# Kernel optimization log

Hardware: AMD Instinct MI355X
Metric: run time of the kernel (lower is better)

The kernel has to match this reference:

```python
import jax, jax.numpy as jnp
import numpy as np

KWTA = 16          # number of winners (kwta)
THRESH = 16384.0   # firing threshold


def setup_inputs() -> dict:
    key = jax.random.key(0)
    k1, k2 = jax.random.split(key)
    # SpykeTorch layout: (timesteps, in_channels, H, W)
    rec_field = jax.random.uniform(k1, (64, 1, 256, 256), dtype=jnp.float32)
    # LocalConvolution weight: kernel covers the full receptive field -> (k, C, kh, kw)
    weight = jax.random.uniform(k2, (2048, 1, 256, 256), dtype=jnp.float32)
    return {"rec_field": rec_field, "weight": weight}


def reference(rec_field, weight):
    T = rec_field.shape[0]
    K = weight.shape[0]
    # LocalConvolution with kernel == receptive field: output spatial dims are 1x1,
    # i.e. a dense projection of the flattened field onto K cells -> (T, K)
    out = jnp.einsum('tchw,kchw->tk', rec_field, weight)
    # sf.fire(out, thresh, True): threshold_ keeps values strictly > thresh, else 0
    pot = jnp.where(out > THRESH, out, jnp.zeros((), out.dtype))  # thresholded potentials
    spikes = jnp.sign(pot)                                        # 0/1 spike wave
    # sf.get_k_winners(pot, kwta, inhibition_radius=0); spikes = pot.sign()
    n_spk = spikes.sum(axis=0)                                    # (K,)
    # index of earliest spike timestep per feature, clamped to [0, T-1]
    first_idx = jnp.clip((T - n_spk).astype(jnp.int32), 0, T - 1)
    first_pot = jnp.take_along_axis(pot, first_idx[None, :], axis=0)  # (1, K)
    trunc = spikes * first_pot                                    # (T, K)
    v = trunc.max() * T                                           # large bias at spike positions
    total = (trunc + spikes * v).sum(axis=0)                      # (K,) ranking score
    # iterative argmax + zeroing of the winning feature (radius 0) == top-k,
    # with the loop's break-on-zero handled by the validity mask
    top_vals, top_idx = jax.lax.top_k(total, KWTA)
    valid = (top_vals > 0).astype(out.dtype)
    coef = jnp.zeros((K,), dtype=out.dtype).at[top_idx].set(valid)  # winner channel mask
    # coef broadcast over timesteps; restore (T, K, 1, 1) spatial layout
    return jnp.sign(pot * coef[None, :])[:, :, None, None]
```

## Files before the change

kernel.cpp:

```cpp
#include <hip/hip_runtime.h>


constexpr int KDIM   = 65536;
constexpr int NCOL   = 2048;
constexpr int TROWS  = 64;
constexpr int CTILE  = 64;
constexpr int KS     = 64;
constexpr int LDW    = KS + 4;
constexpr int KCHUNK = 4096;
constexpr double THRESH = 16384.0;

__global__ __launch_bounds__(256) void gemm_part(const float* __restrict__ A,
                                                 const float* __restrict__ W,
                                                 double* __restrict__ Cacc) {
    __shared__ float As[TROWS][LDW];
    __shared__ float Ws[CTILE][LDW];
    const int tid = threadIdx.x;
    const int cq  = tid & 15;
    const int tq  = tid >> 4;
    const int colBase = blockIdx.x * CTILE;
    const int kBase   = blockIdx.y * KCHUNK;

    double acc[4][4];
#pragma unroll
    for (int i = 0; i < 4; ++i)
#pragma unroll
        for (int c = 0; c < 4; ++c) acc[i][c] = 0.0;

    for (int ck = 0; ck < KCHUNK; ck += KS) {
        const int k0 = kBase + ck;
        __syncthreads();
#pragma unroll
        for (int it = 0; it < 4; ++it) {
            const int f  = (it * 256 + tid) * 4;
            const int r  = f >> 6;
            const int jj = f & 63;
            *(float4*)&As[r][jj] = *(const float4*)(A + (size_t)r * KDIM + k0 + jj);
            *(float4*)&Ws[r][jj] = *(const float4*)(W + (size_t)(colBase + r) * KDIM + k0 + jj);
        }
        __syncthreads();

#pragma unroll 2
        for (int j0 = 0; j0 < KS; j0 += 8) {
            float p[4][4] = {};
#pragma unroll
            for (int h = 0; h < 2; ++h) {
                const int jj = j0 + 4 * h;
                float4 av[4], wv[4];
#pragma unroll
                for (int i = 0; i < 4; ++i) av[i] = *(const float4*)&As[tq + 16 * i][jj];
#pragma unroll
                for (int c = 0; c < 4; ++c) wv[c] = *(const float4*)&Ws[cq + 16 * c][jj];
#pragma unroll
                for (int i = 0; i < 4; ++i)
#pragma unroll
                    for (int c = 0; c < 4; ++c) {
                        p[i][c] = fmaf(av[i].x, wv[c].x, p[i][c]);
                        p[i][c] = fmaf(av[i].y, wv[c].y, p[i][c]);
                        p[i][c] = fmaf(av[i].z, wv[c].z, p[i][c]);
                        p[i][c] = fmaf(av[i].w, wv[c].w, p[i][c]);
                    }
            }
#pragma unroll
            for (int i = 0; i < 4; ++i)
#pragma unroll
                for (int c = 0; c < 4; ++c) acc[i][c] += (double)p[i][c];
        }
    }

#pragma unroll
    for (int i = 0; i < 4; ++i)
#pragma unroll
        for (int c = 0; c < 4; ++c)
            atomicAdd(&Cacc[(size_t)(tq + 16 * i) * NCOL + colBase + cq + 16 * c],
                      acc[i][c]);
}

__global__ __launch_bounds__(256) void colstats(const double* __restrict__ C,
                                                int* __restrict__ nspk,
                                                double* __restrict__ fpot,
                                                unsigned long long* __restrict__ mbits) {
    const int k = blockIdx.x * blockDim.x + threadIdx.x;
    int n = 0;
    for (int t = 0; t < TROWS; ++t) n += (C[(size_t)t * NCOL + k] > THRESH) ? 1 : 0;
    int fi = TROWS - n;
    if (fi > TROWS - 1) fi = TROWS - 1;
    if (fi < 0) fi = 0;
    const double c  = C[(size_t)fi * NCOL + k];
    const double fp = (c > THRESH) ? c : 0.0;
    nspk[k] = n;
    fpot[k] = fp;
    atomicMax(mbits, (unsigned long long)__double_as_longlong(fp));
}

__global__ __launch_bounds__(256) void topk16(const double* __restrict__ fpot,
                                              const int* __restrict__ nspk,
                                              const unsigned long long* __restrict__ mbits,
                                              unsigned int* __restrict__ coef) {
    __shared__ double tot[NCOL];
    __shared__ double bv[256];
    __shared__ int    bi[256];
    const int tid = threadIdx.x;
    const double v = 64.0 * __longlong_as_double((long long)(*mbits));
    for (int k = tid; k < NCOL; k += 256)
        tot[k] = (double)nspk[k] * (fpot[k] + v);
    __syncthreads();

    for (int round = 0; round < 16; ++round) {
        double best  = -1.0;
        int    besti = 1 << 30;
        for (int k = tid; k < NCOL; k += 256) {
            const double t = tot[k];
            if (t > best || (t == best && k < besti)) { best = t; besti = k; }
        }
        bv[tid] = best;
        bi[tid] = besti;
        __syncthreads();
        for (int s = 128; s > 0; s >>= 1) {
            if (tid < s) {
                const double ov = bv[tid + s];
                const int    oi = bi[tid + s];
                if (ov > bv[tid] || (ov == bv[tid] && oi < bi[tid])) {
                    bv[tid] = ov; bi[tid] = oi;
                }
            }
            __syncthreads();
        }
        if (tid == 0) {
            const int w = bi[0];
            if (bv[0] > 0.0) coef[w] = 1u;
            tot[w] = -1.0;
        }
        __syncthreads();
    }
}

__global__ __launch_bounds__(256) void writeout(const double* __restrict__ C,
                                                const unsigned int* __restrict__ coef,
                                                float* __restrict__ out) {
    const int idx = blockIdx.x * blockDim.x + threadIdx.x;
    const int k = idx & (NCOL - 1);
    out[idx] = (coef[k] != 0u && C[idx] > THRESH) ? 1.0f : 0.0f;
}

extern "C" void kernel_launch(void* const* d_in, const int* in_sizes, int n_in,
                              void* d_out, int out_size, void* d_ws, size_t ws_size,
                              hipStream_t stream) {
    (void)in_sizes; (void)n_in; (void)out_size; (void)ws_size;
    const float* A = (const float*)d_in[0];
    const float* W = (const float*)d_in[1];
    float* out = (float*)d_out;

    char* ws = (char*)d_ws;
    double* Cacc = (double*)ws;
    double* fpot = (double*)(ws + 1048576);
    int* nspk    = (int*)(ws + 1048576 + 16384);
    unsigned long long* mbits =
        (unsigned long long*)(ws + 1048576 + 16384 + 8192);
    unsigned int* coef =
        (unsigned int*)(ws + 1048576 + 16384 + 8192 + 8);
    const size_t ws_need = 1048576 + 16384 + 8192 + 8 + 8192;

    hipMemsetAsync(d_ws, 0, ws_need, stream);

    gemm_part<<<dim3(NCOL / CTILE, KDIM / KCHUNK), 256, 0, stream>>>(A, W, Cacc);
    colstats<<<NCOL / 256, 256, 0, stream>>>(Cacc, nspk, fpot, mbits);
    topk16<<<1, 256, 0, stream>>>(fpot, nspk, mbits, coef);
    writeout<<<(TROWS * NCOL) / 256, 256, 0, stream>>>(Cacc, coef, out);
}
```

Before: 929.1 us.

## Replace FP32 FMA GEMM with exact bf16 limb-split MFMA integer accumulation

Inputs are converted to fixed-point integers (scaled by 2^23) and split into three signed 8-bit limbs stored as bf16. Nine cross-limb bf16 MFMA products per tile are accumulated in fp32, then periodically folded into 64-bit integer totals with shifts. The result is an exact integer dot product, so thresholding and top-k ranking run on integers, and ranking uses (spike count, first potential) lexicographically instead of the double-based score. The aim is to move the dominant GEMM onto matrix cores, at the cost of three times the LDS footprint, conversion work per stage, and quantisation of the inputs to 23 fractional bits.

```diff
diff --git a/kernel.cpp b/kernel.cpp
--- a/kernel.cpp
+++ b/kernel.cpp
@@ -1,146 +1,204 @@
 #include <hip/hip_runtime.h>
 
+
+typedef float  f32x4  __attribute__((ext_vector_type(4)));
+typedef __bf16 bf16x8 __attribute__((ext_vector_type(8)));
+typedef short  s16x8  __attribute__((ext_vector_type(8)));
 
 constexpr int KDIM   = 65536;
 constexpr int NCOL   = 2048;
 constexpr int TROWS  = 64;
 constexpr int CTILE  = 64;
 constexpr int KS     = 64;
-constexpr int LDW    = KS + 4;
-constexpr int KCHUNK = 4096;
-constexpr double THRESH = 16384.0;
-
-__global__ __launch_bounds__(256) void gemm_part(const float* __restrict__ A,
-                                                 const float* __restrict__ W,
-                                                 double* __restrict__ Cacc) {
-    __shared__ float As[TROWS][LDW];
-    __shared__ float Ws[CTILE][LDW];
-    const int tid = threadIdx.x;
-    const int cq  = tid & 15;
-    const int tq  = tid >> 4;
+constexpr int SPLIT  = 16;
+constexpr int KRANGE = KDIM / SPLIT;
+constexpr int STAGES = KRANGE / KS;
+constexpr int LDSTR  = 72;
+constexpr long long THRESH_I = 1LL << 60;
+
+__device__ __forceinline__ void convert_write16(const float4 v[4], short* base) {
+    const int PST = TROWS * LDSTR;
+    ushort h[3][16];
+#pragma unroll
+    for (int i = 0; i < 16; ++i) {
+        const float     x  = ((const float*)v)[i];
+        const unsigned  k  = (unsigned)(x * 8388608.0f);
+        const int       d0 = (int)((k + 128u) & 255u) - 128;
+        const unsigned  k1 = (k - (unsigned)d0) >> 8;
+        const int       d1 = (int)((k1 + 128u) & 255u) - 128;
+        const unsigned  k2 = (k1 - (unsigned)d1) >> 8;
+        h[0][i] = (ushort)(__float_as_uint((float)d0) >> 16);
+        h[1][i] = (ushort)(__float_as_uint((float)d1) >> 16);
+        h[2][i] = (ushort)(__float_as_uint((float)(int)k2) >> 16);
+    }
+#pragma unroll
+    for (int p = 0; p < 3; ++p) {
+        s16x8 lo, hi;
+#pragma unroll
+        for (int j = 0; j < 8; ++j) { lo[j] = (short)h[p][j]; hi[j] = (short)h[p][j + 8]; }
+        *(s16x8*)(base + p * PST)     = lo;
+        *(s16x8*)(base + p * PST + 8) = hi;
+    }
+}
+
+__global__ __launch_bounds__(256, 2) void gemm_limb(const float* __restrict__ A,
+                                                    const float* __restrict__ W,
+                                                    unsigned long long* __restrict__ C) {
+    __shared__ short Al[3][TROWS][LDSTR];
+    __shared__ short Wl[3][CTILE][LDSTR];
+    const int tid  = threadIdx.x;
+    const int lane = tid & 63;
+    const int wv   = tid >> 6;
+    const int r0   = (wv >> 1) * 32;
+    const int c0   = (wv & 1) * 32;
     const int colBase = blockIdx.x * CTILE;
-    const int kBase   = blockIdx.y * KCHUNK;
-
-    double acc[4][4];
-#pragma unroll
-    for (int i = 0; i < 4; ++i)
-#pragma unroll
-        for (int c = 0; c < 4; ++c) acc[i][c] = 0.0;
-
-    for (int ck = 0; ck < KCHUNK; ck += KS) {
-        const int k0 = kBase + ck;
-        __syncthreads();
-#pragma unroll
-        for (int it = 0; it < 4; ++it) {
-            const int f  = (it * 256 + tid) * 4;
-            const int r  = f >> 6;
-            const int jj = f & 63;
-            *(float4*)&As[r][jj] = *(const float4*)(A + (size_t)r * KDIM + k0 + jj);
-            *(float4*)&Ws[r][jj] = *(const float4*)(W + (size_t)(colBase + r) * KDIM + k0 + jj);
-        }
-        __syncthreads();
-
-#pragma unroll 2
-        for (int j0 = 0; j0 < KS; j0 += 8) {
-            float p[4][4] = {};
-#pragma unroll
-            for (int h = 0; h < 2; ++h) {
-                const int jj = j0 + 4 * h;
-                float4 av[4], wv[4];
-#pragma unroll
-                for (int i = 0; i < 4; ++i) av[i] = *(const float4*)&As[tq + 16 * i][jj];
-#pragma unroll
-                for (int c = 0; c < 4; ++c) wv[c] = *(const float4*)&Ws[cq + 16 * c][jj];
-#pragma unroll
-                for (int i = 0; i < 4; ++i)
-#pragma unroll
-                    for (int c = 0; c < 4; ++c) {
-                        p[i][c] = fmaf(av[i].x, wv[c].x, p[i][c]);
-                        p[i][c] = fmaf(av[i].y, wv[c].y, p[i][c]);
-                        p[i][c] = fmaf(av[i].z, wv[c].z, p[i][c]);
-                        p[i][c] = fmaf(av[i].w, wv[c].w, p[i][c]);
+    const int kBase   = blockIdx.y * KRANGE;
+
+    const int lrow  = tid >> 2;
+    const int lkoff = (tid & 3) * 16;
+
+    const int frow = lane & 15;
+    const int fk   = (lane >> 4) * 8;
+
+    f32x4 acc[5][2][2] = {};
+    long long tot[2][2][4] = {};
+
+    for (int st = 0; st < STAGES; ++st) {
+        const int k0 = kBase + st * KS;
+        float4 av[4], wv4[4];
+        const float* ap = A + (size_t)lrow * KDIM + k0 + lkoff;
+        const float* wp = W + (size_t)(colBase + lrow) * KDIM + k0 + lkoff;
+#pragma unroll
+        for (int i = 0; i < 4; ++i) av[i] = ((const float4*)ap)[i];
+#pragma unroll
+        for (int i = 0; i < 4; ++i) wv4[i] = ((const float4*)wp)[i];
+
+        __syncthreads();
+        convert_write16(av,  &Al[0][lrow][lkoff]);
+        convert_write16(wv4, &Wl[0][lrow][lkoff]);
+        __syncthreads();
+
+#pragma unroll
+        for (int ks = 0; ks < 2; ++ks) {
+            s16x8 af[3][2], bf[3][2];
+#pragma unroll
+            for (int p = 0; p < 3; ++p)
+#pragma unroll
+                for (int rt = 0; rt < 2; ++rt)
+                    af[p][rt] = *(const s16x8*)&Al[p][r0 + rt * 16 + frow][ks * 32 + fk];
+#pragma unroll
+            for (int p = 0; p < 3; ++p)
+#pragma unroll
+                for (int ct = 0; ct < 2; ++ct)
+                    bf[p][ct] = *(const s16x8*)&Wl[p][c0 + ct * 16 + frow][ks * 32 + fk];
+#pragma unroll
+            for (int p = 0; p < 3; ++p)
+#pragma unroll
+                for (int q = 0; q < 3; ++q) {
+                    const int s = p + q;
+#pragma unroll
+                    for (int rt = 0; rt < 2; ++rt)
+#pragma unroll
+                        for (int ct = 0; ct < 2; ++ct)
+                            acc[s][rt][ct] = __builtin_amdgcn_mfma_f32_16x16x32_bf16(
+                                __builtin_bit_cast(bf16x8, af[p][rt]),
+                                __builtin_bit_cast(bf16x8, bf[q][ct]),
+                                acc[s][rt][ct], 0, 0, 0);
+                }
+        }
+
+        if ((st & 3) == 3) {
+#pragma unroll
+            for (int s = 0; s < 5; ++s)
+#pragma unroll
+                for (int rt = 0; rt < 2; ++rt)
+#pragma unroll
+                    for (int ct = 0; ct < 2; ++ct) {
+#pragma unroll
+                        for (int r = 0; r < 4; ++r)
+                            tot[rt][ct][r] += ((long long)(int)acc[s][rt][ct][r]) << (8 * s);
+                        acc[s][rt][ct] = (f32x4){0.f, 0.f, 0.f, 0.f};
                     }
+        }
+    }
+
+#pragma unroll
+    for (int rt = 0; rt < 2; ++rt)
+#pragma unroll
+        for (int ct = 0; ct < 2; ++ct)
+#pragma unroll
+            for (int r = 0; r < 4; ++r) {
+                const int row = r0 + rt * 16 + (lane >> 4) * 4 + r;
+                const int col = colBase + c0 + ct * 16 + (lane & 15);
+                atomicAdd(&C[(size_t)row * NCOL + col],
+                          (unsigned long long)tot[rt][ct][r]);
             }
-#pragma unroll
-            for (int i = 0; i < 4; ++i)
-#pragma unroll
-                for (int c = 0; c < 4; ++c) acc[i][c] += (double)p[i][c];
-        }
-    }
-
-#pragma unroll
-    for (int i = 0; i < 4; ++i)
-#pragma unroll
-        for (int c = 0; c < 4; ++c)
-            atomicAdd(&Cacc[(size_t)(tq + 16 * i) * NCOL + colBase + cq + 16 * c],
-                      acc[i][c]);
-}
-
-__global__ __launch_bounds__(256) void colstats(const double* __restrict__ C,
+}
+
+__global__ __launch_bounds__(256) void colstats(const long long* __restrict__ C,
                                                 int* __restrict__ nspk,
-                                                double* __restrict__ fpot,
+                                                long long* __restrict__ fpot,
                                                 unsigned long long* __restrict__ mbits) {
     const int k = blockIdx.x * blockDim.x + threadIdx.x;
     int n = 0;
-    for (int t = 0; t < TROWS; ++t) n += (C[(size_t)t * NCOL + k] > THRESH) ? 1 : 0;
+    for (int t = 0; t < TROWS; ++t) n += (C[(size_t)t * NCOL + k] > THRESH_I) ? 1 : 0;
     int fi = TROWS - n;
     if (fi > TROWS - 1) fi = TROWS - 1;
-    if (fi < 0) fi = 0;
-    const double c  = C[(size_t)fi * NCOL + k];
-    const double fp = (c > THRESH) ? c : 0.0;
+    const long long c  = C[(size_t)fi * NCOL + k];
+    const long long fp = (c > THRESH_I) ? c : 0;
     nspk[k] = n;
     fpot[k] = fp;
-    atomicMax(mbits, (unsigned long long)__double_as_longlong(fp));
-}
-
-__global__ __launch_bounds__(256) void topk16(const double* __restrict__ fpot,
+    atomicMax(mbits, (unsigned long long)fp);
+}
+
+__global__ __launch_bounds__(256) void topk16(const long long* __restrict__ fpot,
                                               const int* __restrict__ nspk,
                                               const unsigned long long* __restrict__ mbits,
                                               unsigned int* __restrict__ coef) {
-    __shared__ double tot[NCOL];
-    __shared__ double bv[256];
-    __shared__ int    bi[256];
+    __shared__ long long sf[NCOL];
+    __shared__ int sn[NCOL];
+    __shared__ long long rv[256];
+    __shared__ int rn[256];
+    __shared__ int ri[256];
     const int tid = threadIdx.x;
-    const double v = 64.0 * __longlong_as_double((long long)(*mbits));
-    for (int k = tid; k < NCOL; k += 256)
-        tot[k] = (double)nspk[k] * (fpot[k] + v);
+    const bool anyv = (*mbits) > 0ull;
+    for (int k = tid; k < NCOL; k += 256) { sf[k] = fpot[k]; sn[k] = nspk[k]; }
     __syncthreads();
 
     for (int round = 0; round < 16; ++round) {
-        double best  = -1.0;
-        int    besti = 1 << 30;
+        int bn = -1; long long bf = -1; int bi = 1 << 30;
         for (int k = tid; k < NCOL; k += 256) {
-            const double t = tot[k];
-            if (t > best || (t == best && k < besti)) { best = t; besti = k; }
-        }
-        bv[tid] = best;
-        bi[tid] = besti;
+            const int nn = sn[k]; const long long ff = sf[k];
+            if (nn > bn || (nn == bn && (ff > bf || (ff == bf && k < bi)))) {
+                bn = nn; bf = ff; bi = k;
+            }
+        }
+        rn[tid] = bn; rv[tid] = bf; ri[tid] = bi;
         __syncthreads();
         for (int s = 128; s > 0; s >>= 1) {
             if (tid < s) {
-                const double ov = bv[tid + s];
-                const int    oi = bi[tid + s];
-                if (ov > bv[tid] || (ov == bv[tid] && oi < bi[tid])) {
-                    bv[tid] = ov; bi[tid] = oi;
+                const int on = rn[tid + s]; const long long of = rv[tid + s]; const int oi = ri[tid + s];
+                if (on > rn[tid] || (on == rn[tid] && (of > rv[tid] || (of == rv[tid] && oi < ri[tid])))) {
+                    rn[tid] = on; rv[tid] = of; ri[tid] = oi;
                 }
             }
             __syncthreads();
         }
         if (tid == 0) {
-            const int w = bi[0];
-            if (bv[0] > 0.0) coef[w] = 1u;
-            tot[w] = -1.0;
-        }
-        __syncthreads();
-    }
-}
-
-__global__ __launch_bounds__(256) void writeout(const double* __restrict__ C,
+            const int w = ri[0];
+            if (rn[0] > 0 && anyv) coef[w] = 1u;
+            sn[w] = -1;
+        }
+        __syncthreads();
+    }
+}
+
+__global__ __launch_bounds__(256) void writeout(const long long* __restrict__ C,
                                                 const unsigned int* __restrict__ coef,
                                                 float* __restrict__ out) {
     const int idx = blockIdx.x * blockDim.x + threadIdx.x;
     const int k = idx & (NCOL - 1);
-    out[idx] = (coef[k] != 0u && C[idx] > THRESH) ? 1.0f : 0.0f;
+    out[idx] = (coef[k] != 0u && C[idx] > THRESH_I) ? 1.0f : 0.0f;
 }
 
 extern "C" void kernel_launch(void* const* d_in, const int* in_sizes, int n_in,
@@ -152,18 +210,17 @@
     float* out = (float*)d_out;
 
     char* ws = (char*)d_ws;
-    double* Cacc = (double*)ws;
-    double* fpot = (double*)(ws + 1048576);
-    int* nspk    = (int*)(ws + 1048576 + 16384);
-    unsigned long long* mbits =
-        (unsigned long long*)(ws + 1048576 + 16384 + 8192);
-    unsigned int* coef =
-        (unsigned int*)(ws + 1048576 + 16384 + 8192 + 8);
-    const size_t ws_need = 1048576 + 16384 + 8192 + 8 + 8192;
-
-    hipMemsetAsync(d_ws, 0, ws_need, stream);
-
-    gemm_part<<<dim3(NCOL / CTILE, KDIM / KCHUNK), 256, 0, stream>>>(A, W, Cacc);
+    long long* Cacc = (long long*)ws;
+    unsigned long long* mbits = (unsigned long long*)(ws + 1048576);
+    unsigned int* coef = (unsigned int*)(ws + 1048576 + 8);
+    long long* fpot = (long long*)(ws + 1048576 + 8 + 8192);
+    int* nspk = (int*)(ws + 1048576 + 8 + 8192 + 16384);
+    const size_t zero_bytes = 1048576 + 8 + 8192;
+
+    hipMemsetAsync(d_ws, 0, zero_bytes, stream);
+
+    gemm_limb<<<dim3(NCOL / CTILE, SPLIT), 256, 0, stream>>>(
+        A, W, (unsigned long long*)Cacc);
     colstats<<<NCOL / 256, 256, 0, stream>>>(Cacc, nspk, fpot, mbits);
     topk16<<<1, 256, 0, stream>>>(fpot, nspk, mbits, coef);
     writeout<<<(TROWS * NCOL) / 256, 256, 0, stream>>>(Cacc, coef, out);
```

Result: faster. 849.1 us (-8.6%).
